# Kernel optimization log

Hardware: AMD Instinct MI355X
Metric: run time of the kernel (lower is better)

Reference implementation:

```python
import jax, jax.numpy as jnp
import numpy as np

FEAT_STRIDE = 16
PRE_NMS = 6000
POST_NMS = 300
NMS_THRESH = 0.7


def _whctrs(a):
    w = a[2] - a[0] + 1.0
    h = a[3] - a[1] + 1.0
    return w, h, a[0] + 0.5 * (w - 1), a[1] + 0.5 * (h - 1)

def _mkanchors(ws, hs, xc, yc):
    return np.stack([xc - 0.5 * (ws - 1), yc - 0.5 * (hs - 1),
                     xc + 0.5 * (ws - 1), yc + 0.5 * (hs - 1)], axis=1)

def _ratio_enum(anchor, ratios):
    w, h, xc, yc = _whctrs(anchor)
    size = w * h
    ws = np.round(np.sqrt(size / ratios))
    hs = np.round(ws * ratios)
    return _mkanchors(ws, hs, xc, yc)

def _scale_enum(anchor, scales):
    w, h, xc, yc = _whctrs(anchor)
    return _mkanchors(w * scales, h * scales, xc, yc)

def generate_anchors(base_size=16, ratios=np.array([0.5, 1.0, 2.0]), scales=np.array([8, 16, 32])):
    base = np.array([1, 1, base_size, base_size], dtype=np.float64) - 1
    ra = _ratio_enum(base, np.asarray(ratios, np.float64))
    return np.vstack([_scale_enum(ra[i], np.asarray(scales, np.float64)) for i in range(ra.shape[0])])


def setup_inputs() -> dict:
    key = jax.random.key(0)
    k1, k2 = jax.random.split(key)
    B, A, H, W = 8, 9, 64, 64
    scores = jax.random.normal(k1, (B, 2 * A, H, W), jnp.float32)
    bbox_deltas = jax.random.normal(k2, (B, 4 * A, H, W), jnp.float32)
    anchors = jnp.asarray(generate_anchors(16), jnp.float32)  # [9, 4]
    return {"scores": scores, "bbox_deltas": bbox_deltas, "anchors": anchors,
            "image_width": 1024, "image_height": 1024}


def _nms_keep(iou, thresh):
    # greedy NMS on score-sorted boxes given a full IoU matrix
    n = iou.shape[0]
    idx = jnp.arange(n)
    def body(i, keep):
        sup = keep[i] & (iou[i] > thresh) & (idx > i)
        return keep & ~sup
    return jax.lax.fori_loop(0, n, body, jnp.ones((n,), bool))


def _nms_one(boxes):  # boxes [PRE_NMS, 4], sorted by score desc
    b = jax.lax.stop_gradient(boxes)
    area = (b[:, 2] - b[:, 0] + 1.0) * (b[:, 3] - b[:, 1] + 1.0)
    iw = jnp.clip(jnp.minimum(b[:, None, 2], b[None, :, 2]) -
                  jnp.maximum(b[:, None, 0], b[None, :, 0]) + 1.0, 0.0)
    ih = jnp.clip(jnp.minimum(b[:, None, 3], b[None, :, 3]) -
                  jnp.maximum(b[:, None, 1], b[None, :, 1]) + 1.0, 0.0)
    inter = iw * ih
    iou = inter / (area[:, None] + area[None, :] - inter)
    keep = _nms_keep(iou, NMS_THRESH)
    # compact kept boxes to the front, pad with zeros (fixed shape)
    rank = jnp.cumsum(keep) - 1
    dest = jnp.where(keep, rank, PRE_NMS)  # suppressed -> dump row
    out = jnp.zeros((PRE_NMS + 1, 4), boxes.dtype).at[dest].set(boxes)
    return out[:POST_NMS]


def _forward(scores, bbox_deltas, anchors, image_width, image_height):
    B = scores.shape[0]
    A = anchors.shape[0]
    H, W = scores.shape[2], scores.shape[3]
    fg = scores[:, A:, :, :]                                   # [B, A, H, W]
    # shifted anchor grid
    mx, my = jnp.meshgrid(jnp.arange(W) * FEAT_STRIDE, jnp.arange(H) * FEAT_STRIDE)
    shifts = jnp.stack([mx.ravel(), my.ravel(), mx.ravel(), my.ravel()], 1).astype(scores.dtype)
    all_anchors = (shifts[:, None, :] + anchors[None, :, :]).reshape(-1, 4)  # [K*A, 4]
    deltas = bbox_deltas.transpose(0, 2, 3, 1).reshape(B, -1, 4)             # [B, K*A, 4]
    sc = fg.transpose(0, 2, 3, 1).reshape(B, -1)                             # [B, K*A]
    # bbox_transform_inv
    aw = all_anchors[:, 2] - all_anchors[:, 0] + 1.0
    ah = all_anchors[:, 3] - all_anchors[:, 1] + 1.0
    acx = all_anchors[:, 0] + 0.5 * aw
    acy = all_anchors[:, 1] + 0.5 * ah
    pcx = deltas[..., 0] * aw + acx
    pcy = deltas[..., 1] * ah + acy
    pw = jnp.exp(deltas[..., 2]) * aw
    ph = jnp.exp(deltas[..., 3]) * ah
    # clip to image
    x1 = jnp.clip(pcx - 0.5 * pw, 0.0, image_width - 1)
    y1 = jnp.clip(pcy - 0.5 * ph, 0.0, image_height - 1)
    x2 = jnp.clip(pcx + 0.5 * pw, 0.0, image_width - 1)
    y2 = jnp.clip(pcy + 0.5 * ph, 0.0, image_height - 1)
    proposals = jnp.stack([x1, y1, x2, y2], -1)                 # [B, K*A, 4]
    # per-image pre-NMS top-k by score
    _, order = jax.lax.top_k(sc, PRE_NMS)
    boxes = jnp.take_along_axis(proposals, order[..., None], axis=1)  # [B, PRE, 4]
    props = jax.lax.map(_nms_one, boxes)                        # [B, POST, 4]
    bidx = jnp.broadcast_to(jnp.arange(B, dtype=props.dtype)[:, None, None], (B, POST_NMS, 1))
    return jnp.concatenate([bidx, props], axis=-1)              # [B, POST, 5]


def reference(scores, bbox_deltas, anchors, image_width, image_height):
    return _forward(scores, bbox_deltas, anchors, image_width, image_height)
```

## Files before the change

### kernel.cpp

```cpp
#include <hip/hip_runtime.h>
#include <math.h>

#pragma clang fp contract(off)

#define BB 8
#define AA 9
#define NPIX 4096
#define NN (NPIX*AA)
#define PRE 6000
#define POST 300
#define SELCAP 7000
#define TMAX 10111
#define HZW 5120

#define RA 0x3F000000u
#define RB 0x41000000u
__device__ __forceinline__ unsigned key_bin2(unsigned k) {
    return (k < RA) ? (k >> 17) : (8064u + ((k - RA) >> 14));
}

#define SMEM_BYTES 65536

__device__ __forceinline__ unsigned score_key(float s) {
    unsigned fb = __float_as_uint(s);
    unsigned u = (fb & 0x80000000u) ? ~fb : (fb | 0x80000000u);
    return ~u;
}

__device__ __forceinline__ unsigned phalf(unsigned v, unsigned bin) {
    return (v >> ((bin & 1) << 4)) & 0xFFFFu;
}

__device__ __forceinline__ bool iou_gt(float ax1, float ay1, float ax2, float ay2, float aa,
                                       float bx1_, float by1_, float bx2_, float by2_, float ab) {
    float xx1 = fmaxf(ax1, bx1_);
    float yy1 = fmaxf(ay1, by1_);
    float xx2 = fminf(ax2, bx2_);
    float yy2 = fminf(ay2, by2_);
    float iw = fmaxf(xx2 - xx1 + 1.0f, 0.0f);
    float ih = fmaxf(yy2 - yy1 + 1.0f, 0.0f);
    float inter = iw * ih;
    float uni = (aa + ab) - inter;
    return (double)inter >= 0x1.666667p-1 * (double)uni;
}

__device__ __forceinline__ float area_of(float4 b) {
    return (b.z - b.x + 1.0f) * (b.w - b.y + 1.0f);
}

__device__ __forceinline__ void dec_issue(int g, const unsigned short* sorted16,
                                          const float* anch, const float* deltas_b,
                                          float* aw, float* ah, float* acx, float* acy,
                                          float* d0, float* d1, float* d2, float* d3) {
    unsigned idx = sorted16[(g < PRE) ? g : (PRE - 1)];
    int a = (int)(idx % AA);
    int pix = (int)(idx / AA);
    int wq = pix & 63, hq = pix >> 6;
    float sx = (float)(wq * 16), sy = (float)(hq * 16);
    float ax1 = anch[a * 4 + 0] + sx, ay1 = anch[a * 4 + 1] + sy;
    float ax2 = anch[a * 4 + 2] + sx, ay2 = anch[a * 4 + 3] + sy;
    float w_ = ax2 - ax1 + 1.0f, h_ = ay2 - ay1 + 1.0f;
    *aw = w_; *ah = h_;
    *acx = ax1 + 0.5f * w_; *acy = ay1 + 0.5f * h_;
    const float* dp = deltas_b + (size_t)(a * 4) * NPIX + pix;
    *d0 = dp[0]; *d1 = dp[NPIX]; *d2 = dp[2 * NPIX]; *d3 = dp[3 * NPIX];
}

__device__ __forceinline__ void dec_finish(float aw, float ah, float acx, float acy,
                                           float d0, float d1, float d2, float d3,
                                           float fw, float fh, float4* bx) {
    float pcx = d0 * aw + acx, pcy = d1 * ah + acy;
    float pw = expf(d2) * aw, ph = expf(d3) * ah;
    float x1 = fminf(fmaxf(pcx - 0.5f * pw, 0.0f), fw);
    float y1 = fminf(fmaxf(pcy - 0.5f * ph, 0.0f), fh);
    float x2 = fminf(fmaxf(pcx + 0.5f * pw, 0.0f), fw);
    float y2 = fminf(fmaxf(pcy + 0.5f * ph, 0.0f), fh);
    *bx = make_float4(x1, y1, x2, y2);
}

__device__ __forceinline__ void decode_box(int g, const unsigned short* sorted16,
                                           const float* anch, const float* deltas_b,
                                           float fw, float fh, float4* bx) {
    float aw, ah, acx, acy, d0, d1, d2, d3;
    dec_issue(g, sorted16, anch, deltas_b, &aw, &ah, &acx, &acy, &d0, &d1, &d2, &d3);
    dec_finish(aw, ah, acx, acy, d0, d1, d2, d3, fw, fh, bx);
}

__device__ __forceinline__ void bar_lds() {
    asm volatile("s_waitcnt lgkmcnt(0)" ::: "memory");
    __builtin_amdgcn_s_barrier();
    asm volatile("" ::: "memory");
}

__global__ __launch_bounds__(1024) void proposal_kernel(const float* __restrict__ scores,
                                                        const float* __restrict__ deltas,
                                                        const float* __restrict__ anchors,
                                                        const int* __restrict__ imw,
                                                        const int* __restrict__ imh,
                                                        float* __restrict__ out) {
    __shared__ __align__(16) unsigned char smem[SMEM_BYTES];
    unsigned*       hist32 = (unsigned*)smem;
    unsigned*       keyh   = (unsigned*)(smem + 20480);
    unsigned short* idxl   = (unsigned short*)(smem + 48512);
    unsigned*       scal   = (unsigned*)(smem + 65344);
    unsigned short* sorted16 = (unsigned short*)(smem + 20480);
    float4*         kb4  = (float4*)smem;
    float4*         cnd4 = (float4*)(smem + 4800);
    unsigned long long* srow = (unsigned long long*)(smem + 6848);
    unsigned long long* dkw  = (unsigned long long*)(smem + 7872);
    float*          anch = (float*)(smem + 7904);

    int b = blockIdx.x;
    int tid = threadIdx.x;
    int wave = tid >> 6, lane = tid & 63;
    const float* sc = scores + (size_t)(b * (2 * AA) + AA) * NPIX;
    const float4* sc4 = (const float4*)sc;
    const float* deltas_b = deltas + (size_t)b * (4 * AA) * NPIX;
    float fw = (float)(imw[0] - 1);
    float fh = (float)(imh[0] - 1);

    for (int j = tid; j < HZW; j += 1024) hist32[j] = 0;
    __syncthreads();
    #pragma unroll
    for (int q = 0; q < 9; ++q) {
        float4 v = sc4[(q << 10) + tid];
        unsigned k0 = score_key(v.x), k1 = score_key(v.y);
        unsigned k2 = score_key(v.z), k3 = score_key(v.w);
        if (k0 < RB) { unsigned b0 = key_bin2(k0); atomicAdd(&hist32[b0 >> 1], 1u << ((b0 & 1) << 4)); }
        if (k1 < RB) { unsigned b1 = key_bin2(k1); atomicAdd(&hist32[b1 >> 1], 1u << ((b1 & 1) << 4)); }
        if (k2 < RB) { unsigned b2 = key_bin2(k2); atomicAdd(&hist32[b2 >> 1], 1u << ((b2 & 1) << 4)); }
        if (k3 < RB) { unsigned b3 = key_bin2(k3); atomicAdd(&hist32[b3 >> 1], 1u << ((b3 & 1) << 4)); }
    }
    __syncthreads();

    unsigned ssum = 0;
    const unsigned* hw = hist32 + tid * 16;
    if (tid < 320) {
        #pragma unroll
        for (int j = 0; j < 16; ++j) { unsigned w = hw[j]; ssum += (w & 0xFFFFu) + (w >> 16); }
    }
    unsigned x = ssum;
    #pragma unroll
    for (int d = 1; d < 64; d <<= 1) {
        unsigned y = __shfl_up(x, (unsigned)d, 64);
        if (lane >= d) x += y;
    }
    if (lane == 63 && wave < 5) scal[wave] = x;
    __syncthreads();
    unsigned wexcl = 0;
    #pragma unroll
    for (int w = 0; w < 5; ++w) if (w < wave) wexcl += scal[w];
    unsigned gexcl = wexcl + (x - ssum);
    unsigned gincl = gexcl + ssum;
    if (tid == 319) { scal[16] = TMAX; scal[17] = gincl; }
    __syncthreads();
    if (tid < 320 && gexcl <= (PRE - 1) && (PRE - 1) < gincl) {
        unsigned c = gexcl, T = tid * 32, tot = gincl;
        bool f = false;
        for (int j = 0; j < 32 && !f; ++j) {
            unsigned d = phalf(hw[j >> 1], (unsigned)j);
            if ((PRE - 1) < c + d) { T = tid * 32 + j; tot = c + d; f = true; }
            c += d;
        }
        scal[16] = T;
        scal[17] = tot;
    }
    __syncthreads();
    unsigned T = scal[16];
    if (T > TMAX) T = TMAX;
    unsigned cnt = scal[17];
    if (cnt > SELCAP) cnt = SELCAP;

    if ((unsigned)(tid * 32) <= T) {
        unsigned run = gexcl;
        unsigned* wv = hist32 + tid * 16;
        #pragma unroll
        for (int j = 0; j < 16; ++j) {
            unsigned v = wv[j];
            unsigned c0 = v & 0xFFFFu, c1 = v >> 16;
            wv[j] = run | ((run + c0) << 16);
            run += c0 + c1;
        }
    }
    __syncthreads();

    #pragma unroll
    for (int q = 0; q < 9; ++q) {
        float4 v = sc4[(q << 10) + tid];
        #pragma unroll
        for (int c = 0; c < 4; ++c) {
            float s = (c == 0) ? v.x : (c == 1) ? v.y : (c == 2) ? v.z : v.w;
            unsigned k = score_key(s);
            if (k < RB) {
                unsigned bin = key_bin2(k);
                if (bin <= T) {
                    unsigned old = atomicAdd(&hist32[bin >> 1], 1u << ((bin & 1) << 4));
                    unsigned pos = phalf(old, bin);
                    if (pos < SELCAP) {
                        keyh[pos] = k;
                        int pix = (tid << 2) + c;
                        idxl[pos] = (unsigned short)(pix * AA + q);
                    }
                }
            }
        }
    }
    __syncthreads();

    unsigned rnk8[8], id8[8];
    #pragma unroll
    for (int m = 0; m < 8; ++m) {
        int s = (m << 10) + tid;
        rnk8[m] = 0xFFFFFFFFu;
        if (s < (int)cnt) {
            unsigned k = keyh[s];
            unsigned id = idxl[s];
            unsigned bin = key_bin2(k);
            unsigned start = bin ? phalf(hist32[(bin - 1) >> 1], bin - 1) : 0u;
            unsigned end = phalf(hist32[bin >> 1], bin);
            if (end > cnt) end = cnt;
            if (start > end) start = end;
            unsigned rank = start;
            for (unsigned j = start; j < end; ++j) {
                unsigned kj = keyh[j];
                rank += (kj < k) ? 1u : 0u;
                if (kj == k) rank += ((unsigned)idxl[j] < id) ? 1u : 0u;
            }
            rnk8[m] = rank;
            id8[m] = id;
        }
    }
    __syncthreads();
    #pragma unroll
    for (int m = 0; m < 8; ++m)
        if (rnk8[m] < PRE) sorted16[rnk8[m]] = (unsigned short)id8[m];
    if (tid < 36) anch[tid] = anchors[tid];
    if (tid < 4) dkw[tid] = 0ULL;
    __syncthreads();

    float s_aw = 0.f, s_ah = 0.f, s_acx = 0.f, s_acy = 0.f;
    float s_d0 = 0.f, s_d1 = 0.f, s_d2 = 0.f, s_d3 = 0.f;

    if (tid < 64) {
        float4 bx;
        decode_box(tid, sorted16, anch, deltas_b, fw, fh, &bx);
        cnd4[tid] = bx;
    }
    if (wave == 8)
        dec_issue(64 + lane, sorted16, anch, deltas_b,
                  &s_aw, &s_ah, &s_acx, &s_acy, &s_d0, &s_d1, &s_d2, &s_d3);
    __syncthreads();

    int cur = 0, K = 0, p = 0, pb = 0, rq = 0;
    for (;;) {
        float4 mc = cnd4[p * 64 + lane];
        float ma = area_of(mc);
        float4 cj0 = cnd4[p * 64 + wave];
        float4 cj1 = cnd4[p * 64 + 16 + wave];
        float4 cj2 = cnd4[p * 64 + 32 + wave];
        float4 cj3 = cnd4[p * 64 + 48 + wave];

        if (wave == 8) {
            if (lane == 0) dkw[(rq + 2) & 3] = 0ULL;
            float4 nb;
            dec_finish(s_aw, s_ah, s_acx, s_acy, s_d0, s_d1, s_d2, s_d3,
                       fw, fh, &nb);
            cnd4[(p ^ 1) * 64 + lane] = nb;
            dec_issue(cur + 128 + lane, sorted16, anch, deltas_b,
                      &s_aw, &s_ah, &s_acx, &s_acy, &s_d0, &s_d1, &s_d2, &s_d3);
        }

        bool dead = (cur + lane >= PRE);
        if (wave != 8) {
            int w15 = (wave < 8) ? wave : (wave - 1);
            for (int k = w15; k < K; k += 15) {
                float4 kv = kb4[k];
                dead = dead | iou_gt(kv.x, kv.y, kv.z, kv.w, area_of(kv),
                                     mc.x, mc.y, mc.z, mc.w, ma);
            }
            unsigned long long db = __ballot(dead);
            if (lane == 0) atomicOr(&dkw[rq], db);
        }

        {
            bool g = (lane < wave) && iou_gt(mc.x, mc.y, mc.z, mc.w, ma,
                                             cj0.x, cj0.y, cj0.z, cj0.w, area_of(cj0));
            unsigned long long bl = __ballot(g);
            if (lane == 0) srow[pb * 64 + wave] = bl;
        }
        {
            int j = 16 + wave;
            bool g = (lane < j) && iou_gt(mc.x, mc.y, mc.z, mc.w, ma,
                                          cj1.x, cj1.y, cj1.z, cj1.w, area_of(cj1));
            unsigned long long bl = __ballot(g);
            if (lane == 0) srow[pb * 64 + j] = bl;
        }
        {
            int j = 32 + wave;
            bool g = (lane < j) && iou_gt(mc.x, mc.y, mc.z, mc.w, ma,
                                          cj2.x, cj2.y, cj2.z, cj2.w, area_of(cj2));
            unsigned long long bl = __ballot(g);
            if (lane == 0) srow[pb * 64 + j] = bl;
        }
        {
            int j = 48 + wave;
            bool g = (lane < j) && iou_gt(mc.x, mc.y, mc.z, mc.w, ma,
                                          cj3.x, cj3.y, cj3.z, cj3.w, area_of(cj3));
            unsigned long long bl = __ballot(g);
            if (lane == 0) srow[pb * 64 + j] = bl;
        }

        bar_lds();

        unsigned long long dk = dkw[rq];
        unsigned long long row = srow[pb * 64 + lane];
        unsigned long long live = ~dk;
        unsigned long long keptb = 0ULL;
        int allowed = POST - K;
        while (live) {
            int f = __ffsll((long long)live) - 1;
            keptb |= (1ULL << f);
            if (__popcll(keptb) >= allowed) break;
            bool die = (row >> f) & 1ULL;
            unsigned long long dbl = __ballot(die);
            live &= ~(dbl | (1ULL << f));
        }
        int nkeep = __popcll(keptb);
        int take = (nkeep < allowed) ? nkeep : allowed;

        if ((keptb >> lane) & 1ULL) {
            int rnk = __popcll(keptb & ((1ULL << lane) - 1ULL));
            if (rnk < take) { kb4[K + rnk] = mc; }
        }
        K += take;
        cur += 64;
        if (K >= POST || cur >= PRE) break;
        p ^= 1; pb ^= 1; rq = (rq + 1) & 3;
    }

    __syncthreads();
    for (int idx = tid; idx < POST * 5; idx += 1024) {
        int row_ = idx / 5;
        int col = idx - row_ * 5;
        float val = 0.0f;
        if (row_ < K) {
            float4 v = kb4[row_];
            val = (col == 0) ? (float)b : (col == 1) ? v.x : (col == 2) ? v.y
                : (col == 3) ? v.z : v.w;
        }
        out[(size_t)b * POST * 5 + idx] = val;
    }
}

extern "C" void kernel_launch(void* const* d_in, const int* in_sizes, int n_in,
                              void* d_out, int out_size, void* d_ws, size_t ws_size,
                              hipStream_t stream) {
    const float* scores  = (const float*)d_in[0];
    const float* deltas  = (const float*)d_in[1];
    const float* anchors = (const float*)d_in[2];
    const int*   imw     = (const int*)d_in[3];
    const int*   imh     = (const int*)d_in[4];
    float* out = (float*)d_out;

    proposal_kernel<<<BB, 1024, 0, stream>>>(scores, deltas, anchors, imw, imh, out);
}
```

Before: 140.9 us.

## Process NMS candidates in 128-box chunks with two decode waves

Doubles the NMS step from 64 to 128 candidates per iteration. Each iteration handles two 64-box halves: both halves are tested against kept boxes, and their intra-half suppression rows are built under a single barrier. The second half is additionally checked against boxes kept from the first half using shuffles. Two waves now prefetch and decode the next chunk. This halves the number of block-wide barriers per candidate, but adds a serial cross-half check, doubles per-wave IoU work, and may over-process candidates once 300 boxes are kept.

```diff
diff --git a/kernel.cpp b/kernel.cpp
--- a/kernel.cpp
+++ b/kernel.cpp
@@ -106,9 +106,9 @@
     unsigned short* sorted16 = (unsigned short*)(smem + 20480);
     float4*         kb4  = (float4*)smem;
     float4*         cnd4 = (float4*)(smem + 4800);
-    unsigned long long* srow = (unsigned long long*)(smem + 6848);
-    unsigned long long* dkw  = (unsigned long long*)(smem + 7872);
-    float*          anch = (float*)(smem + 7904);
+    unsigned long long* srow = (unsigned long long*)(smem + 8896);
+    unsigned long long* dkw  = (unsigned long long*)(smem + 10944);
+    float*          anch = (float*)(smem + 11008);
 
     int b = blockIdx.x;
     int tid = threadIdx.x;
@@ -235,105 +235,185 @@
     for (int m = 0; m < 8; ++m)
         if (rnk8[m] < PRE) sorted16[rnk8[m]] = (unsigned short)id8[m];
     if (tid < 36) anch[tid] = anchors[tid];
-    if (tid < 4) dkw[tid] = 0ULL;
+    if (tid < 8) dkw[tid] = 0ULL;
     __syncthreads();
 
     float s_aw = 0.f, s_ah = 0.f, s_acx = 0.f, s_acy = 0.f;
     float s_d0 = 0.f, s_d1 = 0.f, s_d2 = 0.f, s_d3 = 0.f;
 
-    if (tid < 64) {
+    if (tid < 128) {
         float4 bx;
         decode_box(tid, sorted16, anch, deltas_b, fw, fh, &bx);
         cnd4[tid] = bx;
     }
-    if (wave == 8)
-        dec_issue(64 + lane, sorted16, anch, deltas_b,
+    if (wave == 8 || wave == 9)
+        dec_issue(128 + (wave - 8) * 64 + lane, sorted16, anch, deltas_b,
                   &s_aw, &s_ah, &s_acx, &s_acy, &s_d0, &s_d1, &s_d2, &s_d3);
     __syncthreads();
 
     int cur = 0, K = 0, p = 0, pb = 0, rq = 0;
     for (;;) {
-        float4 mc = cnd4[p * 64 + lane];
-        float ma = area_of(mc);
-        float4 cj0 = cnd4[p * 64 + wave];
-        float4 cj1 = cnd4[p * 64 + 16 + wave];
-        float4 cj2 = cnd4[p * 64 + 32 + wave];
-        float4 cj3 = cnd4[p * 64 + 48 + wave];
-
-        if (wave == 8) {
-            if (lane == 0) dkw[(rq + 2) & 3] = 0ULL;
+        float4 mcA = cnd4[p * 128 + lane];
+        float4 mcB = cnd4[p * 128 + 64 + lane];
+        float maA = area_of(mcA);
+        float maB = area_of(mcB);
+        float4 cjA0 = cnd4[p * 128 + wave];
+        float4 cjA1 = cnd4[p * 128 + 16 + wave];
+        float4 cjA2 = cnd4[p * 128 + 32 + wave];
+        float4 cjA3 = cnd4[p * 128 + 48 + wave];
+        float4 cjB0 = cnd4[p * 128 + 64 + wave];
+        float4 cjB1 = cnd4[p * 128 + 80 + wave];
+        float4 cjB2 = cnd4[p * 128 + 96 + wave];
+        float4 cjB3 = cnd4[p * 128 + 112 + wave];
+
+        if (wave == 8 || wave == 9) {
+            if (wave == 8 && lane == 0) {
+                dkw[(rq + 2) & 3] = 0ULL;
+                dkw[4 + ((rq + 2) & 3)] = 0ULL;
+            }
             float4 nb;
             dec_finish(s_aw, s_ah, s_acx, s_acy, s_d0, s_d1, s_d2, s_d3,
                        fw, fh, &nb);
-            cnd4[(p ^ 1) * 64 + lane] = nb;
-            dec_issue(cur + 128 + lane, sorted16, anch, deltas_b,
+            cnd4[(p ^ 1) * 128 + (wave - 8) * 64 + lane] = nb;
+            dec_issue(cur + 256 + (wave - 8) * 64 + lane, sorted16, anch, deltas_b,
                       &s_aw, &s_ah, &s_acx, &s_acy, &s_d0, &s_d1, &s_d2, &s_d3);
         }
 
-        bool dead = (cur + lane >= PRE);
-        if (wave != 8) {
-            int w15 = (wave < 8) ? wave : (wave - 1);
-            for (int k = w15; k < K; k += 15) {
+        if (wave != 8 && wave != 9) {
+            bool deadA = (cur + lane >= PRE);
+            bool deadB = (cur + 64 + lane >= PRE);
+            int w14 = (wave < 8) ? wave : (wave - 2);
+            for (int k = w14; k < K; k += 14) {
                 float4 kv = kb4[k];
-                dead = dead | iou_gt(kv.x, kv.y, kv.z, kv.w, area_of(kv),
-                                     mc.x, mc.y, mc.z, mc.w, ma);
+                float ka = area_of(kv);
+                deadA = deadA | iou_gt(kv.x, kv.y, kv.z, kv.w, ka,
+                                       mcA.x, mcA.y, mcA.z, mcA.w, maA);
+                deadB = deadB | iou_gt(kv.x, kv.y, kv.z, kv.w, ka,
+                                       mcB.x, mcB.y, mcB.z, mcB.w, maB);
             }
-            unsigned long long db = __ballot(dead);
-            if (lane == 0) atomicOr(&dkw[rq], db);
-        }
-
-        {
-            bool g = (lane < wave) && iou_gt(mc.x, mc.y, mc.z, mc.w, ma,
-                                             cj0.x, cj0.y, cj0.z, cj0.w, area_of(cj0));
-            unsigned long long bl = __ballot(g);
-            if (lane == 0) srow[pb * 64 + wave] = bl;
+            unsigned long long dbA = __ballot(deadA);
+            unsigned long long dbB = __ballot(deadB);
+            if (lane == 0) {
+                atomicOr(&dkw[rq], dbA);
+                atomicOr(&dkw[4 + rq], dbB);
+            }
+        }
+
+        {
+            bool g = (lane < wave) && iou_gt(mcA.x, mcA.y, mcA.z, mcA.w, maA,
+                                             cjA0.x, cjA0.y, cjA0.z, cjA0.w, area_of(cjA0));
+            unsigned long long bl = __ballot(g);
+            if (lane == 0) srow[pb * 128 + wave] = bl;
         }
         {
             int j = 16 + wave;
-            bool g = (lane < j) && iou_gt(mc.x, mc.y, mc.z, mc.w, ma,
-                                          cj1.x, cj1.y, cj1.z, cj1.w, area_of(cj1));
-            unsigned long long bl = __ballot(g);
-            if (lane == 0) srow[pb * 64 + j] = bl;
+            bool g = (lane < j) && iou_gt(mcA.x, mcA.y, mcA.z, mcA.w, maA,
+                                          cjA1.x, cjA1.y, cjA1.z, cjA1.w, area_of(cjA1));
+            unsigned long long bl = __ballot(g);
+            if (lane == 0) srow[pb * 128 + j] = bl;
         }
         {
             int j = 32 + wave;
-            bool g = (lane < j) && iou_gt(mc.x, mc.y, mc.z, mc.w, ma,
-                                          cj2.x, cj2.y, cj2.z, cj2.w, area_of(cj2));
-            unsigned long long bl = __ballot(g);
-            if (lane == 0) srow[pb * 64 + j] = bl;
+            bool g = (lane < j) && iou_gt(mcA.x, mcA.y, mcA.z, mcA.w, maA,
+                                          cjA2.x, cjA2.y, cjA2.z, cjA2.w, area_of(cjA2));
+            unsigned long long bl = __ballot(g);
+            if (lane == 0) srow[pb * 128 + j] = bl;
         }
         {
             int j = 48 + wave;
-            bool g = (lane < j) && iou_gt(mc.x, mc.y, mc.z, mc.w, ma,
-                                          cj3.x, cj3.y, cj3.z, cj3.w, area_of(cj3));
-            unsigned long long bl = __ballot(g);
-            if (lane == 0) srow[pb * 64 + j] = bl;
+            bool g = (lane < j) && iou_gt(mcA.x, mcA.y, mcA.z, mcA.w, maA,
+                                          cjA3.x, cjA3.y, cjA3.z, cjA3.w, area_of(cjA3));
+            unsigned long long bl = __ballot(g);
+            if (lane == 0) srow[pb * 128 + j] = bl;
+        }
+        {
+            bool g = (lane < wave) && iou_gt(mcB.x, mcB.y, mcB.z, mcB.w, maB,
+                                             cjB0.x, cjB0.y, cjB0.z, cjB0.w, area_of(cjB0));
+            unsigned long long bl = __ballot(g);
+            if (lane == 0) srow[pb * 128 + 64 + wave] = bl;
+        }
+        {
+            int j = 16 + wave;
+            bool g = (lane < j) && iou_gt(mcB.x, mcB.y, mcB.z, mcB.w, maB,
+                                          cjB1.x, cjB1.y, cjB1.z, cjB1.w, area_of(cjB1));
+            unsigned long long bl = __ballot(g);
+            if (lane == 0) srow[pb * 128 + 64 + j] = bl;
+        }
+        {
+            int j = 32 + wave;
+            bool g = (lane < j) && iou_gt(mcB.x, mcB.y, mcB.z, mcB.w, maB,
+                                          cjB2.x, cjB2.y, cjB2.z, cjB2.w, area_of(cjB2));
+            unsigned long long bl = __ballot(g);
+            if (lane == 0) srow[pb * 128 + 64 + j] = bl;
+        }
+        {
+            int j = 48 + wave;
+            bool g = (lane < j) && iou_gt(mcB.x, mcB.y, mcB.z, mcB.w, maB,
+                                          cjB3.x, cjB3.y, cjB3.z, cjB3.w, area_of(cjB3));
+            unsigned long long bl = __ballot(g);
+            if (lane == 0) srow[pb * 128 + 64 + j] = bl;
         }
 
         bar_lds();
 
-        unsigned long long dk = dkw[rq];
-        unsigned long long row = srow[pb * 64 + lane];
-        unsigned long long live = ~dk;
-        unsigned long long keptb = 0ULL;
+        unsigned long long dkA = dkw[rq];
+        unsigned long long rowA = srow[pb * 128 + lane];
+        unsigned long long rowB = srow[pb * 128 + 64 + lane];
+        unsigned long long dkB0 = dkw[4 + rq];
+        unsigned long long liveA = ~dkA;
+        unsigned long long keptbA = 0ULL;
         int allowed = POST - K;
-        while (live) {
-            int f = __ffsll((long long)live) - 1;
-            keptb |= (1ULL << f);
-            if (__popcll(keptb) >= allowed) break;
-            bool die = (row >> f) & 1ULL;
+        while (liveA) {
+            int f = __ffsll((long long)liveA) - 1;
+            keptbA |= (1ULL << f);
+            if (__popcll(keptbA) >= allowed) break;
+            bool die = (rowA >> f) & 1ULL;
             unsigned long long dbl = __ballot(die);
-            live &= ~(dbl | (1ULL << f));
-        }
-        int nkeep = __popcll(keptb);
-        int take = (nkeep < allowed) ? nkeep : allowed;
-
-        if ((keptb >> lane) & 1ULL) {
-            int rnk = __popcll(keptb & ((1ULL << lane) - 1ULL));
-            if (rnk < take) { kb4[K + rnk] = mc; }
-        }
-        K += take;
-        cur += 64;
+            liveA &= ~(dbl | (1ULL << f));
+        }
+        int nkeepA = __popcll(keptbA);
+        int takeA = (nkeepA < allowed) ? nkeepA : allowed;
+        if ((keptbA >> lane) & 1ULL) {
+            int rnk = __popcll(keptbA & ((1ULL << lane) - 1ULL));
+            if (rnk < takeA) kb4[K + rnk] = mcA;
+        }
+        K += takeA;
+        if (K >= POST) break;
+
+        bool mdead = false;
+        unsigned long long mm = keptbA;
+        for (int t = 0; t < takeA; ++t) {
+            int f = __ffsll((long long)mm) - 1;
+            mm &= mm - 1ULL;
+            float fx1 = __shfl(mcA.x, f);
+            float fy1 = __shfl(mcA.y, f);
+            float fx2 = __shfl(mcA.z, f);
+            float fy2 = __shfl(mcA.w, f);
+            float fa = (fx2 - fx1 + 1.0f) * (fy2 - fy1 + 1.0f);
+            mdead = mdead | iou_gt(fx1, fy1, fx2, fy2, fa,
+                                   mcB.x, mcB.y, mcB.z, mcB.w, maB);
+        }
+        unsigned long long dkB = dkB0 | __ballot(mdead);
+
+        unsigned long long liveB = ~dkB;
+        unsigned long long keptbB = 0ULL;
+        int allowed2 = POST - K;
+        while (liveB) {
+            int f = __ffsll((long long)liveB) - 1;
+            keptbB |= (1ULL << f);
+            if (__popcll(keptbB) >= allowed2) break;
+            bool die = (rowB >> f) & 1ULL;
+            unsigned long long dbl = __ballot(die);
+            liveB &= ~(dbl | (1ULL << f));
+        }
+        int nkeepB = __popcll(keptbB);
+        int takeB = (nkeepB < allowed2) ? nkeepB : allowed2;
+        if ((keptbB >> lane) & 1ULL) {
+            int rnk = __popcll(keptbB & ((1ULL << lane) - 1ULL));
+            if (rnk < takeB) kb4[K + rnk] = mcB;
+        }
+        K += takeB;
+        cur += 128;
         if (K >= POST || cur >= PRE) break;
         p ^= 1; pb ^= 1; rq = (rq + 1) & 3;
     }
```

After: 169.4 us. +20.2%, slower.
